# Kernel optimization log

Measured on AMD Instinct MI355X. Metric: run time of the kernel, lower is better.

Reference implementation:

```python
import jax, jax.numpy as jnp
import numpy as np

C1, C2 = 128, 128

def _glorot(key, shape):
    fan_in = shape[-1]
    return jax.random.normal(key, shape, dtype=jnp.float32) / np.sqrt(fan_in)

def setup_inputs() -> dict:
    key = jax.random.key(0)
    ks = jax.random.split(key, 12)
    b, n = 16, 64
    x = jax.random.normal(ks[0], (b, n, 16), dtype=jnp.float32)
    # 1x1 Conv1d weights stored as [out, in]
    e1_w = _glorot(ks[1], (128, 3));    e1_b = jnp.zeros((128,), jnp.float32)
    e2_w = _glorot(ks[2], (128, 13));   e2_b = jnp.zeros((128,), jnp.float32)
    r1_w = _glorot(ks[3], (256, 128));  r1_b = jnp.zeros((256,), jnp.float32)
    r2_w = _glorot(ks[4], (512, 256));  r2_b = jnp.zeros((512,), jnp.float32)
    r3_w = _glorot(ks[5], (1024, 512)); r3_b = jnp.zeros((1024,), jnp.float32)
    w1   = _glorot(ks[6], (512, 2048)); b1   = jnp.zeros((512,), jnp.float32)
    w2   = _glorot(ks[7], (2048, 512)); b2   = jnp.zeros((2048,), jnp.float32)
    return {"x": x, "e1_w": e1_w, "e1_b": e1_b, "e2_w": e2_w, "e2_b": e2_b,
            "r1_w": r1_w, "r1_b": r1_b, "r2_w": r2_w, "r2_b": r2_b,
            "r3_w": r3_w, "r3_b": r3_b, "w1": w1, "b1": b1, "w2": w2, "b2": b2}

def reference(x, e1_w, e1_b, e2_w, e2_b, r1_w, r1_b, r2_w, r2_b, r3_w, r3_b, w1, b1, w2, b2):
    # x: [b, n, 16]; coord = first 3 dims, pos = last 13 (one-hot-like keypoint id)
    coord, pos = x[:, :, :3], x[:, :, 3:]
    # 1x1 Conv1d == per-point linear. E1/E2 each have their own ReLU, then sum.
    emb = (jax.nn.relu(jnp.einsum('bnc,oc->bno', coord, e1_w) + e1_b)
           + jax.nn.relu(jnp.einsum('bnc,oc->bno', pos, e2_w) + e2_b))  # [b,n,128]
    # refine_E: three 1x1 conv + relu stages -> [b,n,1024]
    emb = jax.nn.relu(jnp.einsum('bnc,oc->bno', emb, r1_w) + r1_b)
    emb = jax.nn.relu(jnp.einsum('bnc,oc->bno', emb, r2_w) + r2_b)
    emb = jax.nn.relu(jnp.einsum('bnc,oc->bno', emb, r3_w) + r3_b)
    # Pairwise layer1: cat((emb_i, emb_j), ch) with emb_i[b,c,i,j]=emb[b,c,j],
    # emb_j[b,c,i,j]=emb[b,c,i]. A 1x1 conv on the concat decomposes into
    # two matmuls applied to emb, broadcast-added pairwise (never forming the
    # [b,2048,n,n] tensor).
    w1a, w1b = w1[:, :1024], w1[:, 1024:]
    A = jnp.einsum('bnc,oc->bno', emb, w1a)  # depends on j
    B = jnp.einsum('bnc,oc->bno', emb, w1b)  # depends on i
    h1 = jax.nn.relu(B[:, :, None, :] + A[:, None, :, :] + b1)  # [b,i,j,512]
    # reduction='mean' over (i,j); layer2 (1x1 conv, linear) commutes with mean
    m = jnp.mean(h1, axis=(1, 2))                 # [b,512]
    out = jnp.einsum('bc,oc->bo', m, w2) + b2     # [b,2048]
    return out
```

## Files before the change

### kernel.cpp

```cpp
#include <hip/hip_runtime.h>


typedef __attribute__((ext_vector_type(8))) short s16x8;
typedef __attribute__((ext_vector_type(8))) unsigned short u16x8;
typedef __attribute__((ext_vector_type(4))) float f32x4;

static __device__ __forceinline__ unsigned short f2bf(float f) {
    unsigned u = __float_as_uint(f);
    u += 0x7fff + ((u >> 16) & 1);
    return (unsigned short)(u >> 16);
}
static __device__ __forceinline__ u16x8 cvt8(float4 a, float4 b) {
    u16x8 r;
    r[0] = f2bf(a.x); r[1] = f2bf(a.y); r[2] = f2bf(a.z); r[3] = f2bf(a.w);
    r[4] = f2bf(b.x); r[5] = f2bf(b.y); r[6] = f2bf(b.z); r[7] = f2bf(b.w);
    return r;
}

__global__ __launch_bounds__(256) void k_embed_gemm1(
    const float* __restrict__ x,
    const float* __restrict__ e1w, const float* __restrict__ e1b,
    const float* __restrict__ e2w, const float* __restrict__ e2b,
    const float* __restrict__ r1w, const float* __restrict__ r1b,
    unsigned short* __restrict__ emb1)
{
    __shared__ float xs[1024];
    __shared__ float e1ws[384], e2ws[1664], e1bs[128], e2bs[128];
    __shared__ unsigned short emb0[64 * 136];
    __shared__ unsigned short Ws[64 * 72];
    int t = threadIdx.x;
    int m0 = blockIdx.x * 64, n0 = blockIdx.y * 64;

    *(float4*)(xs + t * 4) = *(const float4*)(x + (size_t)m0 * 16 + t * 4);
    if (t < 96) *(float4*)(e1ws + t * 4) = *(const float4*)(e1w + t * 4);
    for (int i = t; i < 416; i += 256)
        *(float4*)(e2ws + i * 4) = *(const float4*)(e2w + i * 4);
    if (t < 128) { e1bs[t] = e1b[t]; e2bs[t] = e2b[t]; }
    __syncthreads();
    for (int idx = t; idx < 8192; idx += 256) {
        int rr = idx >> 7, o = idx & 127;
        const float* xr = xs + rr * 16;
        float s1 = e1bs[o] + xr[0] * e1ws[o * 3] + xr[1] * e1ws[o * 3 + 1]
                           + xr[2] * e1ws[o * 3 + 2];
        float s2 = e2bs[o];
#pragma unroll
        for (int k = 0; k < 13; ++k) s2 += xr[3 + k] * e2ws[o * 13 + k];
        emb0[rr * 136 + o] = f2bf(fmaxf(s1, 0.f) + fmaxf(s2, 0.f));
    }

    int lane = t & 63, wv = t >> 6;
    int wm = (wv >> 1) * 32, wn = (wv & 1) * 32;
    int lr = lane & 15, quad = lane >> 4;
    int r = t >> 2, q = (t & 3) * 16;
    const float* wrow = r1w + (size_t)(n0 + r) * 128 + q;
    f32x4 acc[2][2] = {};
    for (int k0 = 0; k0 < 128; k0 += 64) {
        float4 w0 = *(const float4*)(wrow + k0);
        float4 w1v = *(const float4*)(wrow + k0 + 4);
        float4 w2v = *(const float4*)(wrow + k0 + 8);
        float4 w3v = *(const float4*)(wrow + k0 + 12);
        __syncthreads();
        *(u16x8*)(Ws + r * 72 + q)     = cvt8(w0, w1v);
        *(u16x8*)(Ws + r * 72 + q + 8) = cvt8(w2v, w3v);
        __syncthreads();
#pragma unroll
        for (int kk = 0; kk < 64; kk += 32) {
            s16x8 af[2], bf[2];
#pragma unroll
            for (int mt = 0; mt < 2; ++mt)
                af[mt] = *(const s16x8*)(emb0 + (wm + mt * 16 + lr) * 136 + k0 + kk + quad * 8);
#pragma unroll
            for (int nt = 0; nt < 2; ++nt)
                bf[nt] = *(const s16x8*)(Ws + (wn + nt * 16 + lr) * 72 + kk + quad * 8);
#pragma unroll
            for (int mt = 0; mt < 2; ++mt)
#pragma unroll
                for (int nt = 0; nt < 2; ++nt)
                    acc[mt][nt] = __builtin_amdgcn_mfma_f32_16x16x32_bf16(
                        af[mt], bf[nt], acc[mt][nt], 0, 0, 0);
        }
    }
#pragma unroll
    for (int mt = 0; mt < 2; ++mt)
#pragma unroll
        for (int nt = 0; nt < 2; ++nt) {
            int col = n0 + wn + nt * 16 + lr;
            float bv = r1b[col];
#pragma unroll
            for (int rr = 0; rr < 4; ++rr) {
                int row = m0 + wm + mt * 16 + quad * 4 + rr;
                emb1[(size_t)row * 256 + col] = f2bf(fmaxf(acc[mt][nt][rr] + bv, 0.f));
            }
        }
}

__global__ __launch_bounds__(256) void k_gemm(
    const unsigned short* __restrict__ A, const float* __restrict__ Wf,
    const float* __restrict__ bias, unsigned short* __restrict__ Cb,
    int K, int N)
{
    __shared__ unsigned short As[64 * 72];
    __shared__ unsigned short Ws[64 * 72];
    int t = threadIdx.x;
    int m0 = blockIdx.x * 64, n0 = blockIdx.y * 64;
    int lane = t & 63, wv = t >> 6;
    int wm = (wv >> 1) * 32, wn = (wv & 1) * 32;
    int lr = lane & 15, quad = lane >> 4;
    int r = t >> 2, q = (t & 3) * 16;

    const unsigned short* arow = A + (size_t)(m0 + r) * K + q;
    const float* wrow = Wf + (size_t)(n0 + r) * K + q;

    f32x4 acc[2][2] = {};
    for (int k0 = 0; k0 < K; k0 += 64) {
        u16x8 a0 = *(const u16x8*)(arow + k0);
        u16x8 a1 = *(const u16x8*)(arow + k0 + 8);
        float4 w0 = *(const float4*)(wrow + k0);
        float4 w1v = *(const float4*)(wrow + k0 + 4);
        float4 w2v = *(const float4*)(wrow + k0 + 8);
        float4 w3v = *(const float4*)(wrow + k0 + 12);
        __syncthreads();
        *(u16x8*)(As + r * 72 + q)     = a0;
        *(u16x8*)(As + r * 72 + q + 8) = a1;
        *(u16x8*)(Ws + r * 72 + q)     = cvt8(w0, w1v);
        *(u16x8*)(Ws + r * 72 + q + 8) = cvt8(w2v, w3v);
        __syncthreads();
#pragma unroll
        for (int kk = 0; kk < 64; kk += 32) {
            s16x8 af[2], bf[2];
#pragma unroll
            for (int mt = 0; mt < 2; ++mt)
                af[mt] = *(const s16x8*)(As + (wm + mt * 16 + lr) * 72 + kk + quad * 8);
#pragma unroll
            for (int nt = 0; nt < 2; ++nt)
                bf[nt] = *(const s16x8*)(Ws + (wn + nt * 16 + lr) * 72 + kk + quad * 8);
#pragma unroll
            for (int mt = 0; mt < 2; ++mt)
#pragma unroll
                for (int nt = 0; nt < 2; ++nt)
                    acc[mt][nt] = __builtin_amdgcn_mfma_f32_16x16x32_bf16(
                        af[mt], bf[nt], acc[mt][nt], 0, 0, 0);
        }
    }
#pragma unroll
    for (int mt = 0; mt < 2; ++mt)
#pragma unroll
        for (int nt = 0; nt < 2; ++nt) {
            int col = n0 + wn + nt * 16 + lr;
            float bv = bias[col];
#pragma unroll
            for (int rr = 0; rr < 4; ++rr) {
                int row = m0 + wm + mt * 16 + quad * 4 + rr;
                Cb[(size_t)row * N + col] = f2bf(fmaxf(acc[mt][nt][rr] + bv, 0.f));
            }
        }
}

__global__ __launch_bounds__(256) void k_gemm4_pair(
    const unsigned short* __restrict__ emb3, const float* __restrict__ w1,
    const float* __restrict__ b1, float* __restrict__ msum)
{
    __shared__ unsigned short As[64 * 72];
    __shared__ unsigned short Ws[128 * 72];
    __shared__ float sA[64 * 68];
    __shared__ float sB[64 * 68];
    int t = threadIdx.x;
    int cb = blockIdx.x, b = blockIdx.y;
    int lane = t & 63, wv = t >> 6;
    int wn = wv * 32;
    int lr = lane & 15, quad = lane >> 4;

    int r = t >> 2, q = (t & 3) * 16;
    const unsigned short* arow = emb3 + (size_t)(b * 64 + r) * 1024 + q;
    int rw = t >> 1, qw = (t & 1) * 32;
    const float* wrow = w1 + (size_t)(cb * 64 + (rw & 63)) * 2048
                           + ((rw >= 64) ? 1024 : 0) + qw;

    f32x4 acc[4][2] = {};
    for (int k0 = 0; k0 < 1024; k0 += 64) {
        u16x8 a0 = *(const u16x8*)(arow + k0);
        u16x8 a1 = *(const u16x8*)(arow + k0 + 8);
        float4 f0 = *(const float4*)(wrow + k0);
        float4 f1 = *(const float4*)(wrow + k0 + 4);
        float4 f2 = *(const float4*)(wrow + k0 + 8);
        float4 f3 = *(const float4*)(wrow + k0 + 12);
        float4 f4 = *(const float4*)(wrow + k0 + 16);
        float4 f5 = *(const float4*)(wrow + k0 + 20);
        float4 f6 = *(const float4*)(wrow + k0 + 24);
        float4 f7 = *(const float4*)(wrow + k0 + 28);
        __syncthreads();
        *(u16x8*)(As + r * 72 + q)       = a0;
        *(u16x8*)(As + r * 72 + q + 8)   = a1;
        *(u16x8*)(Ws + rw * 72 + qw)      = cvt8(f0, f1);
        *(u16x8*)(Ws + rw * 72 + qw + 8)  = cvt8(f2, f3);
        *(u16x8*)(Ws + rw * 72 + qw + 16) = cvt8(f4, f5);
        *(u16x8*)(Ws + rw * 72 + qw + 24) = cvt8(f6, f7);
        __syncthreads();
#pragma unroll
        for (int kk = 0; kk < 64; kk += 32) {
            s16x8 af[4], bf[2];
#pragma unroll
            for (int mt = 0; mt < 4; ++mt)
                af[mt] = *(const s16x8*)(As + (mt * 16 + lr) * 72 + kk + quad * 8);
#pragma unroll
            for (int nt = 0; nt < 2; ++nt)
                bf[nt] = *(const s16x8*)(Ws + (wn + nt * 16 + lr) * 72 + kk + quad * 8);
#pragma unroll
            for (int mt = 0; mt < 4; ++mt)
#pragma unroll
                for (int nt = 0; nt < 2; ++nt)
                    acc[mt][nt] = __builtin_amdgcn_mfma_f32_16x16x32_bf16(
                        af[mt], bf[nt], acc[mt][nt], 0, 0, 0);
        }
    }

#pragma unroll
    for (int mt = 0; mt < 4; ++mt)
#pragma unroll
        for (int nt = 0; nt < 2; ++nt) {
            int col = wn + nt * 16 + lr;
            float* dst = (col < 64) ? sA : sB;
            int c = col & 63;
#pragma unroll
            for (int rr = 0; rr < 4; ++rr)
                dst[(mt * 16 + quad * 4 + rr) * 68 + c] = acc[mt][nt][rr];
        }
    __syncthreads();

    {
        int c = t & 63, ig = t >> 6;
        float b1c = b1[cb * 64 + c];
        float bv[16];
#pragma unroll
        for (int i = 0; i < 16; ++i) bv[i] = sB[(ig * 16 + i) * 68 + c] + b1c;
        float s = 0.f;
        for (int j = 0; j < 64; ++j) {
            float a = sA[j * 68 + c];
#pragma unroll
            for (int i = 0; i < 16; ++i) s += fmaxf(bv[i] + a, 0.f);
        }
        float* sPart = (float*)As;
        sPart[ig * 64 + c] = s;
        __syncthreads();
        if (t < 64)
            msum[b * 512 + cb * 64 + t] =
                sPart[t] + sPart[64 + t] + sPart[128 + t] + sPart[192 + t];
    }
}

__global__ __launch_bounds__(256) void k_final(
    const float* __restrict__ msum, const float* __restrict__ w2,
    const float* __restrict__ b2, float* __restrict__ out)
{
    __shared__ float sm[512];
    int t = threadIdx.x;
    int b = blockIdx.x;
    int o = blockIdx.y * 256 + t;
    sm[t]       = msum[b * 512 + t]       * (1.f / 4096.f);
    sm[t + 256] = msum[b * 512 + 256 + t] * (1.f / 4096.f);
    __syncthreads();
    const float* wr = w2 + (size_t)o * 512;
    float acc = 0.f;
#pragma unroll 8
    for (int c = 0; c < 512; c += 4) {
        float4 w = *(const float4*)(wr + c);
        acc += sm[c] * w.x + sm[c + 1] * w.y + sm[c + 2] * w.z + sm[c + 3] * w.w;
    }
    out[b * 2048 + o] = acc + b2[o];
}

extern "C" void kernel_launch(void* const* d_in, const int* in_sizes, int n_in,
                              void* d_out, int out_size, void* d_ws, size_t ws_size,
                              hipStream_t stream)
{
    const float* x   = (const float*)d_in[0];
    const float* e1w = (const float*)d_in[1];
    const float* e1b = (const float*)d_in[2];
    const float* e2w = (const float*)d_in[3];
    const float* e2b = (const float*)d_in[4];
    const float* r1w = (const float*)d_in[5];
    const float* r1b = (const float*)d_in[6];
    const float* r2w = (const float*)d_in[7];
    const float* r2b = (const float*)d_in[8];
    const float* r3w = (const float*)d_in[9];
    const float* r3b = (const float*)d_in[10];
    const float* w1  = (const float*)d_in[11];
    const float* b1  = (const float*)d_in[12];
    const float* w2  = (const float*)d_in[13];
    const float* b2  = (const float*)d_in[14];
    float* out = (float*)d_out;

    unsigned short* emb1 = (unsigned short*)d_ws;
    unsigned short* emb2 = emb1 + 1024 * 256;
    unsigned short* emb3 = emb2 + 1024 * 512;
    float* msum = (float*)(emb3 + 1024 * 1024);

    k_embed_gemm1<<<dim3(16, 4), 256, 0, stream>>>(x, e1w, e1b, e2w, e2b,
                                                   r1w, r1b, emb1);
    k_gemm<<<dim3(16, 8),  256, 0, stream>>>(emb1, r2w, r2b, emb2, 256, 512);
    k_gemm<<<dim3(16, 16), 256, 0, stream>>>(emb2, r3w, r3b, emb3, 512, 1024);
    k_gemm4_pair<<<dim3(8, 16), 256, 0, stream>>>(emb3, w1, b1, msum);
    k_final<<<dim3(16, 8), 256, 0, stream>>>(msum, w2, b2, out);
}
```

Before: 161.1 us.

## Pre-convert weights to bf16 once per call and retile pairwise GEMM

Adds a kernel that converts r2w, r3w and w1 to bf16 (reordering w1 into [1024,1024]) before the GEMMs. The GEMM kernels then load bf16 weights directly instead of converting fp32 tiles in every block, which halves weight bytes per load and removes repeated conversion across M-blocks. The pairwise kernel is retiled to 32 output channels per block with a 2x2 wave layout, doubling its grid to 256 blocks for better occupancy. The cost is an extra launch plus a full read and write of the weights each call.

```diff
diff --git a/kernel.cpp b/kernel.cpp
--- a/kernel.cpp
+++ b/kernel.cpp
@@ -15,6 +15,27 @@
     r[0] = f2bf(a.x); r[1] = f2bf(a.y); r[2] = f2bf(a.z); r[3] = f2bf(a.w);
     r[4] = f2bf(b.x); r[5] = f2bf(b.y); r[6] = f2bf(b.z); r[7] = f2bf(b.w);
     return r;
+}
+
+__global__ __launch_bounds__(256) void k_convw(
+    const float* __restrict__ r2w, const float* __restrict__ r3w,
+    const float* __restrict__ w1,
+    unsigned short* __restrict__ r2wb, unsigned short* __restrict__ r3wb,
+    unsigned short* __restrict__ w1b)
+{
+    const int n1 = 512 * 256, n2 = 1024 * 512;
+    int i = (blockIdx.x * 256 + threadIdx.x) * 4;
+    float4 v; unsigned short* dst; int j;
+    if (i < n1)           { j = i;        v = *(const float4*)(r2w + j); dst = r2wb + j; }
+    else if (i < n1 + n2) { j = i - n1;   v = *(const float4*)(r3w + j); dst = r3wb + j; }
+    else {
+        j = i - n1 - n2;
+        int n = j >> 10, k = j & 1023;
+        v = *(const float4*)(w1 + (size_t)(n & 511) * 2048 + (n >> 9) * 1024 + k);
+        dst = w1b + j;
+    }
+    ushort4 o; o.x = f2bf(v.x); o.y = f2bf(v.y); o.z = f2bf(v.z); o.w = f2bf(v.w);
+    *(ushort4*)dst = o;
 }
 
 __global__ __launch_bounds__(256) void k_embed_gemm1(
@@ -95,7 +116,7 @@
 }
 
 __global__ __launch_bounds__(256) void k_gemm(
-    const unsigned short* __restrict__ A, const float* __restrict__ Wf,
+    const unsigned short* __restrict__ A, const unsigned short* __restrict__ W,
     const float* __restrict__ bias, unsigned short* __restrict__ Cb,
     int K, int N)
 {
@@ -109,21 +130,19 @@
     int r = t >> 2, q = (t & 3) * 16;
 
     const unsigned short* arow = A + (size_t)(m0 + r) * K + q;
-    const float* wrow = Wf + (size_t)(n0 + r) * K + q;
+    const unsigned short* wrow = W + (size_t)(n0 + r) * K + q;
 
     f32x4 acc[2][2] = {};
     for (int k0 = 0; k0 < K; k0 += 64) {
         u16x8 a0 = *(const u16x8*)(arow + k0);
         u16x8 a1 = *(const u16x8*)(arow + k0 + 8);
-        float4 w0 = *(const float4*)(wrow + k0);
-        float4 w1v = *(const float4*)(wrow + k0 + 4);
-        float4 w2v = *(const float4*)(wrow + k0 + 8);
-        float4 w3v = *(const float4*)(wrow + k0 + 12);
+        u16x8 w0 = *(const u16x8*)(wrow + k0);
+        u16x8 w1 = *(const u16x8*)(wrow + k0 + 8);
         __syncthreads();
         *(u16x8*)(As + r * 72 + q)     = a0;
         *(u16x8*)(As + r * 72 + q + 8) = a1;
-        *(u16x8*)(Ws + r * 72 + q)     = cvt8(w0, w1v);
-        *(u16x8*)(Ws + r * 72 + q + 8) = cvt8(w2v, w3v);
+        *(u16x8*)(Ws + r * 72 + q)     = w0;
+        *(u16x8*)(Ws + r * 72 + q + 8) = w1;
         __syncthreads();
 #pragma unroll
         for (int kk = 0; kk < 64; kk += 32) {
@@ -157,56 +176,48 @@
 }
 
 __global__ __launch_bounds__(256) void k_gemm4_pair(
-    const unsigned short* __restrict__ emb3, const float* __restrict__ w1,
+    const unsigned short* __restrict__ emb3, const unsigned short* __restrict__ w1b,
     const float* __restrict__ b1, float* __restrict__ msum)
 {
     __shared__ unsigned short As[64 * 72];
-    __shared__ unsigned short Ws[128 * 72];
-    __shared__ float sA[64 * 68];
-    __shared__ float sB[64 * 68];
+    __shared__ unsigned short Ws[64 * 72];
+    __shared__ float sA[64 * 36];
+    __shared__ float sB[64 * 36];
     int t = threadIdx.x;
     int cb = blockIdx.x, b = blockIdx.y;
+    int c0 = cb * 32;
     int lane = t & 63, wv = t >> 6;
-    int wn = wv * 32;
+    int wm = (wv >> 1) * 32, wn = (wv & 1) * 32;
     int lr = lane & 15, quad = lane >> 4;
-
     int r = t >> 2, q = (t & 3) * 16;
+
     const unsigned short* arow = emb3 + (size_t)(b * 64 + r) * 1024 + q;
-    int rw = t >> 1, qw = (t & 1) * 32;
-    const float* wrow = w1 + (size_t)(cb * 64 + (rw & 63)) * 2048
-                           + ((rw >= 64) ? 1024 : 0) + qw;
-
-    f32x4 acc[4][2] = {};
+    int wrn = (r < 32) ? (c0 + r) : (512 + c0 + r - 32);
+    const unsigned short* wrow = w1b + (size_t)wrn * 1024 + q;
+
+    f32x4 acc[2][2] = {};
     for (int k0 = 0; k0 < 1024; k0 += 64) {
         u16x8 a0 = *(const u16x8*)(arow + k0);
         u16x8 a1 = *(const u16x8*)(arow + k0 + 8);
-        float4 f0 = *(const float4*)(wrow + k0);
-        float4 f1 = *(const float4*)(wrow + k0 + 4);
-        float4 f2 = *(const float4*)(wrow + k0 + 8);
-        float4 f3 = *(const float4*)(wrow + k0 + 12);
-        float4 f4 = *(const float4*)(wrow + k0 + 16);
-        float4 f5 = *(const float4*)(wrow + k0 + 20);
-        float4 f6 = *(const float4*)(wrow + k0 + 24);
-        float4 f7 = *(const float4*)(wrow + k0 + 28);
-        __syncthreads();
-        *(u16x8*)(As + r * 72 + q)       = a0;
-        *(u16x8*)(As + r * 72 + q + 8)   = a1;
-        *(u16x8*)(Ws + rw * 72 + qw)      = cvt8(f0, f1);
-        *(u16x8*)(Ws + rw * 72 + qw + 8)  = cvt8(f2, f3);
-        *(u16x8*)(Ws + rw * 72 + qw + 16) = cvt8(f4, f5);
-        *(u16x8*)(Ws + rw * 72 + qw + 24) = cvt8(f6, f7);
+        u16x8 w0 = *(const u16x8*)(wrow + k0);
+        u16x8 w1 = *(const u16x8*)(wrow + k0 + 8);
+        __syncthreads();
+        *(u16x8*)(As + r * 72 + q)     = a0;
+        *(u16x8*)(As + r * 72 + q + 8) = a1;
+        *(u16x8*)(Ws + r * 72 + q)     = w0;
+        *(u16x8*)(Ws + r * 72 + q + 8) = w1;
         __syncthreads();
 #pragma unroll
         for (int kk = 0; kk < 64; kk += 32) {
-            s16x8 af[4], bf[2];
-#pragma unroll
-            for (int mt = 0; mt < 4; ++mt)
-                af[mt] = *(const s16x8*)(As + (mt * 16 + lr) * 72 + kk + quad * 8);
+            s16x8 af[2], bf[2];
+#pragma unroll
+            for (int mt = 0; mt < 2; ++mt)
+                af[mt] = *(const s16x8*)(As + (wm + mt * 16 + lr) * 72 + kk + quad * 8);
 #pragma unroll
             for (int nt = 0; nt < 2; ++nt)
                 bf[nt] = *(const s16x8*)(Ws + (wn + nt * 16 + lr) * 72 + kk + quad * 8);
 #pragma unroll
-            for (int mt = 0; mt < 4; ++mt)
+            for (int mt = 0; mt < 2; ++mt)
 #pragma unroll
                 for (int nt = 0; nt < 2; ++nt)
                     acc[mt][nt] = __builtin_amdgcn_mfma_f32_16x16x32_bf16(
@@ -214,37 +225,41 @@
         }
     }
 
-#pragma unroll
-    for (int mt = 0; mt < 4; ++mt)
+    __syncthreads();
+#pragma unroll
+    for (int mt = 0; mt < 2; ++mt)
 #pragma unroll
         for (int nt = 0; nt < 2; ++nt) {
             int col = wn + nt * 16 + lr;
-            float* dst = (col < 64) ? sA : sB;
-            int c = col & 63;
+            float* dst = (col < 32) ? sA : sB;
+            int c = col & 31;
 #pragma unroll
             for (int rr = 0; rr < 4; ++rr)
-                dst[(mt * 16 + quad * 4 + rr) * 68 + c] = acc[mt][nt][rr];
+                dst[(wm + mt * 16 + quad * 4 + rr) * 36 + c] = acc[mt][nt][rr];
         }
     __syncthreads();
 
     {
-        int c = t & 63, ig = t >> 6;
-        float b1c = b1[cb * 64 + c];
-        float bv[16];
-#pragma unroll
-        for (int i = 0; i < 16; ++i) bv[i] = sB[(ig * 16 + i) * 68 + c] + b1c;
+        int c = t & 31, ig = t >> 5;
+        float b1c = b1[c0 + c];
+        float bv[8];
+#pragma unroll
+        for (int i = 0; i < 8; ++i) bv[i] = sB[(ig * 8 + i) * 36 + c] + b1c;
         float s = 0.f;
         for (int j = 0; j < 64; ++j) {
-            float a = sA[j * 68 + c];
-#pragma unroll
-            for (int i = 0; i < 16; ++i) s += fmaxf(bv[i] + a, 0.f);
+            float a = sA[j * 36 + c];
+#pragma unroll
+            for (int i = 0; i < 8; ++i) s += fmaxf(bv[i] + a, 0.f);
         }
         float* sPart = (float*)As;
-        sPart[ig * 64 + c] = s;
-        __syncthreads();
-        if (t < 64)
-            msum[b * 512 + cb * 64 + t] =
-                sPart[t] + sPart[64 + t] + sPart[128 + t] + sPart[192 + t];
+        sPart[ig * 32 + c] = s;
+        __syncthreads();
+        if (t < 32) {
+            float tot = 0.f;
+#pragma unroll
+            for (int i = 0; i < 8; ++i) tot += sPart[i * 32 + t];
+            msum[b * 512 + c0 + t] = tot;
+        }
     }
 }
 
@@ -293,12 +308,16 @@
     unsigned short* emb1 = (unsigned short*)d_ws;
     unsigned short* emb2 = emb1 + 1024 * 256;
     unsigned short* emb3 = emb2 + 1024 * 512;
-    float* msum = (float*)(emb3 + 1024 * 1024);
-
+    unsigned short* r2wb = emb3 + 1024 * 1024;
+    unsigned short* r3wb = r2wb + 512 * 256;
+    unsigned short* w1b  = r3wb + 1024 * 512;
+    float* msum = (float*)(w1b + 1024 * 1024);
+
+    k_convw<<<1664, 256, 0, stream>>>(r2w, r3w, w1, r2wb, r3wb, w1b);
     k_embed_gemm1<<<dim3(16, 4), 256, 0, stream>>>(x, e1w, e1b, e2w, e2b,
                                                    r1w, r1b, emb1);
-    k_gemm<<<dim3(16, 8),  256, 0, stream>>>(emb1, r2w, r2b, emb2, 256, 512);
-    k_gemm<<<dim3(16, 16), 256, 0, stream>>>(emb2, r3w, r3b, emb3, 512, 1024);
-    k_gemm4_pair<<<dim3(8, 16), 256, 0, stream>>>(emb3, w1, b1, msum);
+    k_gemm<<<dim3(16, 8),  256, 0, stream>>>(emb1, r2wb, r2b, emb2, 256, 512);
+    k_gemm<<<dim3(16, 16), 256, 0, stream>>>(emb2, r3wb, r3b, emb3, 512, 1024);
+    k_gemm4_pair<<<dim3(16, 16), 256, 0, stream>>>(emb3, w1b, b1, msum);
     k_final<<<dim3(16, 8), 256, 0, stream>>>(msum, w2, b2, out);
 }
```

New measurement: 140.0 us. 13.1% less time.
